# Kernel tuning notes

Hardware: AMD Instinct MI355X
Metric: run time of the kernel (lower is better)

Reference implementation:

```python
import jax, jax.numpy as jnp
import numpy as np

B, N, D = 4, 2048, 1024
H = 16
HD = D // H  # head_dim = 64
SCALE = HD ** -0.5


def setup_inputs() -> dict:
    key = jax.random.key(0)
    k1, k2, k3, k4 = jax.random.split(key, 4)
    x = jax.random.normal(k1, (B, N, D), dtype=jnp.float32)
    # init-scale weights for numerically sane softmax logits
    w_qkv = jax.random.normal(k2, (3 * D, D), dtype=jnp.float32) * 0.02
    w_proj = jax.random.normal(k3, (D, D), dtype=jnp.float32) * 0.02
    b_proj = jax.random.normal(k4, (D,), dtype=jnp.float32) * 0.02
    return {"x": x, "w_qkv": w_qkv, "w_proj": w_proj, "b_proj": b_proj}


def reference(x, w_qkv, w_proj, b_proj):
    # qkv projection (width_mult=1.0 -> Dyna slicing is identity; qkv_bias=False)
    qkv = jnp.einsum('bnd,ed->bne', x, w_qkv)          # (B, N, 3D)
    qkv = qkv.reshape(B, N, 3, H, HD)
    q = qkv[:, :, 0].transpose(0, 2, 1, 3)              # (B, H, N, HD)
    k = qkv[:, :, 1].transpose(0, 2, 1, 3)
    v = qkv[:, :, 2].transpose(0, 2, 1, 3)
    q = q * SCALE
    attn = jnp.einsum('bhqd,bhkd->bhqk', q, k)          # (B, H, N, N)
    attn = jax.nn.softmax(attn, axis=-1)
    out = jnp.einsum('bhqk,bhkd->bhqd', attn, v)        # (B, H, N, HD)
    out = out.transpose(0, 2, 1, 3).reshape(B, N, D)
    # output projection (bias=True)
    return jnp.einsum('bnd,ed->bne', out, w_proj) + b_proj
```

## Files before the change

kernel.cpp:

```cpp
#include <hip/hip_runtime.h>
#include <hip/hip_bf16.h>
#include <stdint.h>


typedef __attribute__((ext_vector_type(8))) short short8;
typedef __attribute__((ext_vector_type(4))) short short4v;
typedef __attribute__((ext_vector_type(4))) float float4v;

#define MFMA16(a, b, c) __builtin_amdgcn_mfma_f32_16x16x32_bf16((a), (b), (c), 0, 0, 0)
#define MFMA16K16(a, b, c) __builtin_amdgcn_mfma_f32_16x16x16bf16_1k((a), (b), (c), 0, 0, 0)

static __device__ __forceinline__ unsigned short f2bf(float f) {
  union { float f; unsigned u; } v; v.f = f;
  unsigned r = v.u + 0x7fffu + ((v.u >> 16) & 1u);
  return (unsigned short)(r >> 16);
}
static __device__ __forceinline__ float bf2f(unsigned short u) {
  union { unsigned u; float f; } v; v.u = ((unsigned)u) << 16;
  return v.f;
}
static __device__ __forceinline__ unsigned pkbf(float a, float b) {
  union { __hip_bfloat162 v; unsigned u; } c;
  c.v = __float22bfloat162_rn(make_float2(a, b));
  return c.u;
}
static __device__ __forceinline__ float ex2(float x) {
#if __has_builtin(__builtin_amdgcn_exp2f)
  return __builtin_amdgcn_exp2f(x);
#else
  return exp2f(x);
#endif
}
static __device__ __forceinline__ float4v fzero() {
  float4v z; z[0] = 0.f; z[1] = 0.f; z[2] = 0.f; z[3] = 0.f; return z;
}
static __device__ __forceinline__ void load_lds16(const void* g, void* l) {
  typedef const __attribute__((address_space(1))) void* gp_t;
  typedef __attribute__((address_space(3))) void* lp_t;
  __builtin_amdgcn_global_load_lds((gp_t)(uintptr_t)g, (lp_t)(uint32_t)(uintptr_t)l, 16, 0, 0);
}

__global__ void detect_dtype(const unsigned short* __restrict__ x, int* flag) {
  __shared__ int cnt;
  if (threadIdx.x == 0) cnt = 0;
  __syncthreads();
  int c = 0;
  for (int i = threadIdx.x; i < 4096; i += 256) {
    const unsigned v = x[i] & 0x7FFFu;
    if ((v >> 7) >= 134u) ++c;
  }
  atomicAdd(&cnt, c);
  __syncthreads();
  if (threadIdx.x == 0) *flag = (cnt > 64) ? 1 : 0;
}

static __device__ __forceinline__ void cv8(const void* src, unsigned short* dst,
                                           int i, int fl) {
  if (fl) {
    const float* s = (const float*)src + i;
    short8 o;
    for (int j = 0; j < 8; ++j) o[j] = (short)f2bf(s[j]);
    *(short8*)(dst + i) = o;
  } else {
    *(short8*)(dst + i) = *(const short8*)((const unsigned short*)src + i);
  }
}
__global__ __launch_bounds__(256) void convert_all(
    const void* __restrict__ s0, const void* __restrict__ s1,
    const void* __restrict__ s2, const void* __restrict__ s3,
    unsigned short* __restrict__ d0, unsigned short* __restrict__ d1,
    unsigned short* __restrict__ d2, unsigned short* __restrict__ d3,
    const int* __restrict__ flag) {
  const int t = blockIdx.x * 256 + threadIdx.x;
  const int fl = *flag;
  if (t < 1048576)       cv8(s0, d0, t * 8, fl);
  else if (t < 1441792)  cv8(s1, d1, (t - 1048576) * 8, fl);
  else if (t < 1572864)  cv8(s2, d2, (t - 1441792) * 8, fl);
  else if (t < 1572992)  cv8(s3, d3, (t - 1572864) * 8, fl);
}

__global__ __launch_bounds__(256) void qkv_gemm(
    const unsigned short* __restrict__ X, const unsigned short* __restrict__ W,
    unsigned short* __restrict__ Qo, unsigned short* __restrict__ Ko,
    unsigned short* __restrict__ Vt) {
  __shared__ __attribute__((aligned(16))) unsigned short lA[128 * 32];
  __shared__ __attribute__((aligned(16))) unsigned short lB[128 * 32];
  const int tid = threadIdx.x;
  const int wave = tid >> 6, lane = tid & 63, quad = lane >> 4, l16 = lane & 15;
  const int wm = wave >> 1, wn = wave & 1;
  const int m0 = blockIdx.x * 128, n0 = blockIdx.y * 128;

  float4v acc[4][4];
  for (int i = 0; i < 4; ++i) for (int j = 0; j < 4; ++j) acc[i][j] = fzero();

  const int f0 = tid, f1 = 256 + tid;
  const int r0 = f0 >> 2, c0 = (f0 & 3) * 8;
  const int r1 = f1 >> 2, c1 = (f1 & 3) * 8;
  unsigned short* dA0 = lA + (wave * 64) * 8;
  unsigned short* dA1 = lA + (256 + wave * 64) * 8;
  unsigned short* dB0 = lB + (wave * 64) * 8;
  unsigned short* dB1 = lB + (256 + wave * 64) * 8;

  for (int k0 = 0; k0 < 1024; k0 += 32) {
    __syncthreads();
    load_lds16(X + (size_t)(m0 + r0) * 1024 + k0 + c0, dA0);
    load_lds16(X + (size_t)(m0 + r1) * 1024 + k0 + c1, dA1);
    load_lds16(W + (size_t)(n0 + r0) * 1024 + k0 + c0, dB0);
    load_lds16(W + (size_t)(n0 + r1) * 1024 + k0 + c1, dB1);
    __syncthreads();
    short8 af[4], bfr[4];
    for (int t = 0; t < 4; ++t) {
      af[t]  = *(const short8*)(lA + (wm * 64 + t * 16 + l16) * 32 + quad * 8);
      bfr[t] = *(const short8*)(lB + (wn * 64 + t * 16 + l16) * 32 + quad * 8);
    }
    for (int mt = 0; mt < 4; ++mt)
      for (int nt = 0; nt < 4; ++nt)
        acc[mt][nt] = MFMA16(af[mt], bfr[nt], acc[mt][nt]);
  }

  const float QSCALE = 0.18033688011112042f;
  for (int mt = 0; mt < 4; ++mt) {
    const int mbase = m0 + wm * 64 + mt * 16 + quad * 4;
    const int b = mbase >> 11;
    const int nrow = mbase & 2047;
    for (int nt = 0; nt < 4; ++nt) {
      const int e = n0 + wn * 64 + nt * 16 + l16;
      const int c = e >> 10, h = (e >> 6) & 15, hd = e & 63;
      const int bh = b * 16 + h;
      if (c == 0) {
        for (int r = 0; r < 4; ++r)
          Qo[((size_t)bh * 2048 + nrow + r) * 64 + hd] = f2bf(acc[mt][nt][r] * QSCALE);
      } else if (c == 1) {
        for (int r = 0; r < 4; ++r)
          Ko[((size_t)bh * 2048 + nrow + r) * 64 + hd] = f2bf(acc[mt][nt][r]);
      } else {
        short4v pk;
        for (int r = 0; r < 4; ++r) pk[r] = (short)f2bf(acc[mt][nt][r]);
        *(short4v*)(Vt + ((size_t)bh * 64 + hd) * 2048 + nrow) = pk;
      }
    }
  }
}

__global__ __launch_bounds__(256, 4) void flash_attn(
    const unsigned short* __restrict__ Q, const unsigned short* __restrict__ K,
    const unsigned short* __restrict__ Vt, unsigned short* __restrict__ AO) {
  __shared__ __attribute__((aligned(16))) unsigned short lK[2][64 * 72];
  __shared__ __attribute__((aligned(16))) unsigned short lV[2][64 * 72];
  const int tid = threadIdx.x;
  const int wave = tid >> 6, lane = tid & 63, quad = lane >> 4, l16 = lane & 15;
  const int qt = blockIdx.x, bh = blockIdx.y;
  const int b = bh >> 4, h = bh & 15;
  const size_t base = (size_t)bh * 2048 * 64;
  const unsigned short* Qp = Q + base;
  const unsigned short* Kp = K + base;
  const unsigned short* Vp = Vt + base;
  const int q0 = qt * 128;

  const int qa = q0 + wave * 16 + l16;
  const short8 qfA0 = *(const short8*)(Qp + (size_t)qa * 64 + quad * 8);
  const short8 qfA1 = *(const short8*)(Qp + (size_t)qa * 64 + 32 + quad * 8);
  const short8 qfB0 = *(const short8*)(Qp + (size_t)(qa + 64) * 64 + quad * 8);
  const short8 qfB1 = *(const short8*)(Qp + (size_t)(qa + 64) * 64 + 32 + quad * 8);

  float4v oaccA[4], oaccB[4];
  for (int i = 0; i < 4; ++i) { oaccA[i] = fzero(); oaccB[i] = fzero(); }
  float lsumA = 0.f, lsumB = 0.f;

  const int f0 = tid, f1 = 256 + tid;
  const int sk0 = (f0 >> 3) * 72 + (f0 & 7) * 8;
  const int sk1 = (f1 >> 3) * 72 + (f1 & 7) * 8;

  short8 kv0 = *(const short8*)(Kp + f0 * 8);
  short8 kv1 = *(const short8*)(Kp + f1 * 8);
  short8 vv0 = *(const short8*)(Vp + (size_t)(f0 >> 3) * 2048 + (f0 & 7) * 8);
  short8 vv1 = *(const short8*)(Vp + (size_t)(f1 >> 3) * 2048 + (f1 & 7) * 8);

  for (int kb = 0; kb < 32; ++kb) {
    unsigned short* const Kb = lK[kb & 1];
    unsigned short* const Vb = lV[kb & 1];
    *(short8*)(Kb + sk0) = kv0;
    *(short8*)(Kb + sk1) = kv1;
    *(short8*)(Vb + sk0) = vv0;
    *(short8*)(Vb + sk1) = vv1;
    __syncthreads();
    if (kb < 31) {
      const size_t ko = (size_t)(kb + 1) * 4096;
      kv0 = *(const short8*)(Kp + ko + f0 * 8);
      kv1 = *(const short8*)(Kp + ko + f1 * 8);
      vv0 = *(const short8*)(Vp + (size_t)(f0 >> 3) * 2048 + (kb + 1) * 64 + (f0 & 7) * 8);
      vv1 = *(const short8*)(Vp + (size_t)(f1 >> 3) * 2048 + (kb + 1) * 64 + (f1 & 7) * 8);
    }

#pragma unroll
    for (int t = 0; t < 4; ++t) {
      const short8 k0f = *(const short8*)(Kb + (t * 16 + l16) * 72 + quad * 8);
      const short8 k1f = *(const short8*)(Kb + (t * 16 + l16) * 72 + 32 + quad * 8);
      float4v sA = MFMA16(k0f, qfA0, fzero());
      sA = MFMA16(k1f, qfA1, sA);
      float4v sB = MFMA16(k0f, qfB0, fzero());
      sB = MFMA16(k1f, qfB1, sB);

      const float eA0 = ex2(sA[0]), eA1 = ex2(sA[1]);
      const float eA2 = ex2(sA[2]), eA3 = ex2(sA[3]);
      const float eB0 = ex2(sB[0]), eB1 = ex2(sB[1]);
      const float eB2 = ex2(sB[2]), eB3 = ex2(sB[3]);
      lsumA += (eA0 + eA1) + (eA2 + eA3);
      lsumB += (eB0 + eB1) + (eB2 + eB3);
      union { unsigned u[2]; short4v s; } ca, cb;
      ca.u[0] = pkbf(eA0, eA1); ca.u[1] = pkbf(eA2, eA3);
      cb.u[0] = pkbf(eB0, eB1); cb.u[1] = pkbf(eB2, eB3);

      const unsigned short* vrow = Vb + l16 * 72 + quad * 4 + t * 16;
#pragma unroll
      for (int nt = 0; nt < 4; ++nt) {
        const short4v vf = *(const short4v*)(vrow + nt * 16 * 72);
        oaccA[nt] = MFMA16K16(vf, ca.s, oaccA[nt]);
        oaccB[nt] = MFMA16K16(vf, cb.s, oaccB[nt]);
      }
    }
  }

  lsumA += __shfl_xor(lsumA, 16); lsumA += __shfl_xor(lsumA, 32);
  lsumB += __shfl_xor(lsumB, 16); lsumB += __shfl_xor(lsumB, 32);
  const float invA = 1.f / lsumA, invB = 1.f / lsumB;

  unsigned short* aoA = AO + ((size_t)(b * 2048 + qa)) * 1024 + h * 64 + quad * 4;
  unsigned short* aoB = aoA + (size_t)64 * 1024;
  for (int nt = 0; nt < 4; ++nt) {
    union { unsigned u[2]; short4v s; } oa, ob;
    oa.u[0] = pkbf(oaccA[nt][0] * invA, oaccA[nt][1] * invA);
    oa.u[1] = pkbf(oaccA[nt][2] * invA, oaccA[nt][3] * invA);
    ob.u[0] = pkbf(oaccB[nt][0] * invB, oaccB[nt][1] * invB);
    ob.u[1] = pkbf(oaccB[nt][2] * invB, oaccB[nt][3] * invB);
    *(short4v*)(aoA + nt * 16) = oa.s;
    *(short4v*)(aoB + nt * 16) = ob.s;
  }
}

__global__ __launch_bounds__(256) void proj_gemm(
    const unsigned short* __restrict__ A, const unsigned short* __restrict__ W,
    const unsigned short* __restrict__ bias_bf, const void* __restrict__ bias_raw,
    void* __restrict__ outv, const int* __restrict__ flag) {
  __shared__ __attribute__((aligned(16))) unsigned short lA[128 * 32];
  __shared__ __attribute__((aligned(16))) unsigned short lB[128 * 32];
  const int tid = threadIdx.x;
  const int wave = tid >> 6, lane = tid & 63, quad = lane >> 4, l16 = lane & 15;
  const int wm = wave >> 1, wn = wave & 1;
  const int m0 = blockIdx.x * 128, n0 = blockIdx.y * 128;
  const int fl = *flag;

  float4v acc[4][4];
  for (int i = 0; i < 4; ++i) for (int j = 0; j < 4; ++j) acc[i][j] = fzero();

  const int f0 = tid, f1 = 256 + tid;
  const int r0 = f0 >> 2, c0 = (f0 & 3) * 8;
  const int r1 = f1 >> 2, c1 = (f1 & 3) * 8;
  unsigned short* dA0 = lA + (wave * 64) * 8;
  unsigned short* dA1 = lA + (256 + wave * 64) * 8;
  unsigned short* dB0 = lB + (wave * 64) * 8;
  unsigned short* dB1 = lB + (256 + wave * 64) * 8;

  for (int k0 = 0; k0 < 1024; k0 += 32) {
    __syncthreads();
    load_lds16(A + (size_t)(m0 + r0) * 1024 + k0 + c0, dA0);
    load_lds16(A + (size_t)(m0 + r1) * 1024 + k0 + c1, dA1);
    load_lds16(W + (size_t)(n0 + r0) * 1024 + k0 + c0, dB0);
    load_lds16(W + (size_t)(n0 + r1) * 1024 + k0 + c1, dB1);
    __syncthreads();
    short8 af[4], bfr[4];
    for (int t = 0; t < 4; ++t) {
      af[t]  = *(const short8*)(lA + (wm * 64 + t * 16 + l16) * 32 + quad * 8);
      bfr[t] = *(const short8*)(lB + (wn * 64 + t * 16 + l16) * 32 + quad * 8);
    }
    for (int mt = 0; mt < 4; ++mt)
      for (int nt = 0; nt < 4; ++nt)
        acc[mt][nt] = MFMA16(af[mt], bfr[nt], acc[mt][nt]);
  }

  for (int mt = 0; mt < 4; ++mt) {
    const int mbase = m0 + wm * 64 + mt * 16 + quad * 4;
    for (int nt = 0; nt < 4; ++nt) {
      const int e = n0 + wn * 64 + nt * 16 + l16;
      const float bv = fl ? ((const float*)bias_raw)[e] : bf2f(bias_bf[e]);
      for (int r = 0; r < 4; ++r) {
        const float val = acc[mt][nt][r] + bv;
        const size_t idx = (size_t)(mbase + r) * 1024 + e;
        if (fl) ((float*)outv)[idx] = val;
        else    ((unsigned short*)outv)[idx] = f2bf(val);
      }
    }
  }
}

extern "C" void kernel_launch(void* const* d_in, const int* in_sizes, int n_in,
                              void* d_out, int out_size, void* d_ws, size_t ws_size,
                              hipStream_t stream) {
  const void* x_raw     = d_in[0];
  const void* wqkv_raw  = d_in[1];
  const void* wproj_raw = d_in[2];
  const void* bproj_raw = d_in[3];

  const size_t NE = (size_t)4 * 16 * 2048 * 64;
  unsigned short* ws = (unsigned short*)d_ws;
  unsigned short* Q      = ws;
  unsigned short* K      = Q + NE;
  unsigned short* Vt     = K + NE;
  unsigned short* xb     = Vt + NE;
  unsigned short* AO     = xb;
  unsigned short* wqkvb  = xb + NE;
  unsigned short* wprojb = wqkvb + 3145728;
  unsigned short* bprojb = wprojb + 1048576;
  int* flag = (int*)(bprojb + 1024);

  detect_dtype<<<1, 256, 0, stream>>>((const unsigned short*)x_raw, flag);
  convert_all<<<6145, 256, 0, stream>>>(x_raw, wqkv_raw, wproj_raw, bproj_raw,
                                        xb, wqkvb, wprojb, bprojb, flag);

  qkv_gemm<<<dim3(64, 24), 256, 0, stream>>>(xb, wqkvb, Q, K, Vt);
  flash_attn<<<dim3(16, 64), 256, 0, stream>>>(Q, K, Vt, AO);
  proj_gemm<<<dim3(64, 8), 256, 0, stream>>>(AO, wprojb, bprojb, bproj_raw,
                                             d_out, flag);
}
```

Baseline: 285.8 us.

## Double-buffer LDS tiles in QKV and projection GEMMs; vectorize fp32 conversion loads

Both GEMM kernels now use two LDS buffers and issue the global-to-LDS load for the next K tile before the MFMAs on the current tile. This is meant to hide global load latency behind compute and drops one barrier per iteration. LDS use per block doubles, which may reduce occupancy. The fp32-to-bf16 conversion kernel also reads its input as two float4 vectors instead of eight scalar loads. The single remaining barrier relies on load_lds16 completing before it; if that helper is asynchronous without a wait, the prefetch could race with readers.

```diff
diff --git a/kernel.cpp b/kernel.cpp
--- a/kernel.cpp
+++ b/kernel.cpp
@@ -57,9 +57,13 @@
 static __device__ __forceinline__ void cv8(const void* src, unsigned short* dst,
                                            int i, int fl) {
   if (fl) {
-    const float* s = (const float*)src + i;
+    const float4v a = *(const float4v*)((const float*)src + i);
+    const float4v b = *(const float4v*)((const float*)src + i + 4);
     short8 o;
-    for (int j = 0; j < 8; ++j) o[j] = (short)f2bf(s[j]);
+    o[0] = (short)f2bf(a[0]); o[1] = (short)f2bf(a[1]);
+    o[2] = (short)f2bf(a[2]); o[3] = (short)f2bf(a[3]);
+    o[4] = (short)f2bf(b[0]); o[5] = (short)f2bf(b[1]);
+    o[6] = (short)f2bf(b[2]); o[7] = (short)f2bf(b[3]);
     *(short8*)(dst + i) = o;
   } else {
     *(short8*)(dst + i) = *(const short8*)((const unsigned short*)src + i);
@@ -83,8 +87,8 @@
     const unsigned short* __restrict__ X, const unsigned short* __restrict__ W,
     unsigned short* __restrict__ Qo, unsigned short* __restrict__ Ko,
     unsigned short* __restrict__ Vt) {
-  __shared__ __attribute__((aligned(16))) unsigned short lA[128 * 32];
-  __shared__ __attribute__((aligned(16))) unsigned short lB[128 * 32];
+  __shared__ __attribute__((aligned(16))) unsigned short lA[2][128 * 32];
+  __shared__ __attribute__((aligned(16))) unsigned short lB[2][128 * 32];
   const int tid = threadIdx.x;
   const int wave = tid >> 6, lane = tid & 63, quad = lane >> 4, l16 = lane & 15;
   const int wm = wave >> 1, wn = wave & 1;
@@ -96,27 +100,32 @@
   const int f0 = tid, f1 = 256 + tid;
   const int r0 = f0 >> 2, c0 = (f0 & 3) * 8;
   const int r1 = f1 >> 2, c1 = (f1 & 3) * 8;
-  unsigned short* dA0 = lA + (wave * 64) * 8;
-  unsigned short* dA1 = lA + (256 + wave * 64) * 8;
-  unsigned short* dB0 = lB + (wave * 64) * 8;
-  unsigned short* dB1 = lB + (256 + wave * 64) * 8;
-
+  const int dof0 = (wave * 64) * 8;
+  const int dof1 = (256 + wave * 64) * 8;
+
+#define QKV_STAGE(buf, k0)                                                   \
+  load_lds16(X + (size_t)(m0 + r0) * 1024 + (k0) + c0, lA[buf] + dof0);      \
+  load_lds16(X + (size_t)(m0 + r1) * 1024 + (k0) + c1, lA[buf] + dof1);      \
+  load_lds16(W + (size_t)(n0 + r0) * 1024 + (k0) + c0, lB[buf] + dof0);      \
+  load_lds16(W + (size_t)(n0 + r1) * 1024 + (k0) + c1, lB[buf] + dof1);
+
+  QKV_STAGE(0, 0);
+  __syncthreads();
+  int cur = 0;
   for (int k0 = 0; k0 < 1024; k0 += 32) {
-    __syncthreads();
-    load_lds16(X + (size_t)(m0 + r0) * 1024 + k0 + c0, dA0);
-    load_lds16(X + (size_t)(m0 + r1) * 1024 + k0 + c1, dA1);
-    load_lds16(W + (size_t)(n0 + r0) * 1024 + k0 + c0, dB0);
-    load_lds16(W + (size_t)(n0 + r1) * 1024 + k0 + c1, dB1);
-    __syncthreads();
+    if (k0 < 992) { QKV_STAGE(cur ^ 1, k0 + 32); }
     short8 af[4], bfr[4];
     for (int t = 0; t < 4; ++t) {
-      af[t]  = *(const short8*)(lA + (wm * 64 + t * 16 + l16) * 32 + quad * 8);
-      bfr[t] = *(const short8*)(lB + (wn * 64 + t * 16 + l16) * 32 + quad * 8);
+      af[t]  = *(const short8*)(lA[cur] + (wm * 64 + t * 16 + l16) * 32 + quad * 8);
+      bfr[t] = *(const short8*)(lB[cur] + (wn * 64 + t * 16 + l16) * 32 + quad * 8);
     }
     for (int mt = 0; mt < 4; ++mt)
       for (int nt = 0; nt < 4; ++nt)
         acc[mt][nt] = MFMA16(af[mt], bfr[nt], acc[mt][nt]);
-  }
+    __syncthreads();
+    cur ^= 1;
+  }
+#undef QKV_STAGE
 
   const float QSCALE = 0.18033688011112042f;
   for (int mt = 0; mt < 4; ++mt) {
@@ -242,8 +251,8 @@
     const unsigned short* __restrict__ A, const unsigned short* __restrict__ W,
     const unsigned short* __restrict__ bias_bf, const void* __restrict__ bias_raw,
     void* __restrict__ outv, const int* __restrict__ flag) {
-  __shared__ __attribute__((aligned(16))) unsigned short lA[128 * 32];
-  __shared__ __attribute__((aligned(16))) unsigned short lB[128 * 32];
+  __shared__ __attribute__((aligned(16))) unsigned short lA[2][128 * 32];
+  __shared__ __attribute__((aligned(16))) unsigned short lB[2][128 * 32];
   const int tid = threadIdx.x;
   const int wave = tid >> 6, lane = tid & 63, quad = lane >> 4, l16 = lane & 15;
   const int wm = wave >> 1, wn = wave & 1;
@@ -256,27 +265,32 @@
   const int f0 = tid, f1 = 256 + tid;
   const int r0 = f0 >> 2, c0 = (f0 & 3) * 8;
   const int r1 = f1 >> 2, c1 = (f1 & 3) * 8;
-  unsigned short* dA0 = lA + (wave * 64) * 8;
-  unsigned short* dA1 = lA + (256 + wave * 64) * 8;
-  unsigned short* dB0 = lB + (wave * 64) * 8;
-  unsigned short* dB1 = lB + (256 + wave * 64) * 8;
-
+  const int dof0 = (wave * 64) * 8;
+  const int dof1 = (256 + wave * 64) * 8;
+
+#define PROJ_STAGE(buf, k0)                                                  \
+  load_lds16(A + (size_t)(m0 + r0) * 1024 + (k0) + c0, lA[buf] + dof0);      \
+  load_lds16(A + (size_t)(m0 + r1) * 1024 + (k0) + c1, lA[buf] + dof1);     \
+  load_lds16(W + (size_t)(n0 + r0) * 1024 + (k0) + c0, lB[buf] + dof0);      \
+  load_lds16(W + (size_t)(n0 + r1) * 1024 + (k0) + c1, lB[buf] + dof1);
+
+  PROJ_STAGE(0, 0);
+  __syncthreads();
+  int cur = 0;
   for (int k0 = 0; k0 < 1024; k0 += 32) {
-    __syncthreads();
-    load_lds16(A + (size_t)(m0 + r0) * 1024 + k0 + c0, dA0);
-    load_lds16(A + (size_t)(m0 + r1) * 1024 + k0 + c1, dA1);
-    load_lds16(W + (size_t)(n0 + r0) * 1024 + k0 + c0, dB0);
-    load_lds16(W + (size_t)(n0 + r1) * 1024 + k0 + c1, dB1);
-    __syncthreads();
+    if (k0 < 992) { PROJ_STAGE(cur ^ 1, k0 + 32); }
     short8 af[4], bfr[4];
     for (int t = 0; t < 4; ++t) {
-      af[t]  = *(const short8*)(lA + (wm * 64 + t * 16 + l16) * 32 + quad * 8);
-      bfr[t] = *(const short8*)(lB + (wn * 64 + t * 16 + l16) * 32 + quad * 8);
+      af[t]  = *(const short8*)(lA[cur] + (wm * 64 + t * 16 + l16) * 32 + quad * 8);
+      bfr[t] = *(const short8*)(lB[cur] + (wn * 64 + t * 16 + l16) * 32 + quad * 8);
     }
     for (int mt = 0; mt < 4; ++mt)
       for (int nt = 0; nt < 4; ++nt)
         acc[mt][nt] = MFMA16(af[mt], bfr[nt], acc[mt][nt]);
-  }
+    __syncthreads();
+    cur ^= 1;
+  }
+#undef PROJ_STAGE
 
   for (int mt = 0; mt < 4; ++mt) {
     const int mbase = m0 + wm * 64 + mt * 16 + quad * 4;
```

Measured after the change: 271.2 us. 1.05x faster.
